# Kernel optimization log

Hardware: AMD Instinct MI355X
Metric: run time of the kernel (lower is better)

## Reference

```python
import jax, jax.numpy as jnp
import numpy as np

B, N = 32, 512
N_DIM, N_P, N_K = 128, 3, 2
F0_DIM = N_DIM * N_P            # 384
CAT_DIM = N_DIM * (N_K + 1) * N_P  # 1152


def setup_inputs() -> dict:
    key = jax.random.key(0)
    ks = jax.random.split(key, 12)
    s = 0.05
    return {
        "loc": jax.random.uniform(ks[0], (B, N, 2), dtype=jnp.float32),
        "deadline": jax.random.uniform(ks[1], (B, N), dtype=jnp.float32),
        "workload": jax.random.uniform(ks[2], (B, N), dtype=jnp.float32),
        "depot": jax.random.uniform(ks[3], (B, 1, 2), dtype=jnp.float32),
        "W_init": jax.random.normal(ks[4], (3, F0_DIM), dtype=jnp.float32) * s,
        "b_init": jnp.zeros((F0_DIM,), jnp.float32),
        "W_dep": jax.random.normal(ks[5], (2, N_DIM), dtype=jnp.float32) * s,
        "b_dep": jnp.zeros((N_DIM,), jnp.float32),
        "W_g1": jax.random.normal(ks[6], (CAT_DIM, N_DIM), dtype=jnp.float32) * s,
        "b_g1": jnp.zeros((N_DIM,), jnp.float32),
        "W_g2": jax.random.normal(ks[7], (CAT_DIM, N_DIM), dtype=jnp.float32) * s,
        "b_g2": jnp.zeros((N_DIM,), jnp.float32),
        "W_g3": jax.random.normal(ks[8], (CAT_DIM, N_DIM), dtype=jnp.float32) * s,
        "b_g3": jnp.zeros((N_DIM,), jnp.float32),
        "gamma": jnp.ones((F0_DIM,), jnp.float32),
        "beta": jnp.zeros((F0_DIM,), jnp.float32),
        "W_F": jax.random.normal(ks[9], (F0_DIM, N_DIM), dtype=jnp.float32) * s,
        "b_F": jnp.zeros((N_DIM,), jnp.float32),
    }


def _forward(loc, deadline, workload, depot, W_init, b_init, W_dep, b_dep,
             W_g1, b_g1, W_g2, b_g2, W_g3, b_g3, gamma, beta, W_F, b_F):
    # X = [loc, deadline/deadline.max()] -> [B,N,3] (workload is concatenated then dropped in original)
    X = jnp.concatenate([loc, (deadline / deadline.max())[..., None]], axis=-1)
    n = X.shape[1]
    # pairwise squared distances [B,N,N]
    d2 = ((X[:, :, None, :] - X[:, None, :, :]) ** 2).sum(-1)
    off = ~jnp.eye(n, dtype=bool)                      # off-diagonal mask
    d2_safe = jnp.where(off, d2, 1.0)
    A = jnp.where(off, 1.0 / jnp.sqrt(d2_safe), 0.0)   # A = 1/dist off-diag, 0 on diag
    A = jnp.where(jnp.isnan(A), 0.0, A)                # A[A!=A]=0
    A = A / A.max()                                    # global max-normalize
    deg = A.sum(-1) - 1.0                              # (A.sum(-1) - 1)
    L = jnp.eye(n, dtype=A.dtype) * deg[:, None, :] - A  # D - A (diag = deg)
    L2 = L @ L

    F0 = X @ W_init + b_init                           # [B,N,384]
    F0_sq = F0 * F0
    F0_cu = F0 * F0_sq

    def prop(F):
        return jnp.concatenate([F, L @ F, L2 @ F], axis=-1)  # [B,N,1152]

    g1 = prop(F0) @ W_g1 + b_g1
    g2 = prop(F0_sq) @ W_g2 + b_g2
    g3 = prop(F0_cu) @ W_g3 + b_g3
    F1 = jnp.concatenate([g1, g2, g3], axis=-1)        # [B,N,384]
    F1 = jax.nn.leaky_relu(F1) + F0

    # BatchNorm1d (training mode): stats over flattened (B*N) samples, biased var
    flat = F1.reshape(-1, F1.shape[-1])
    mu = flat.mean(0)
    var = ((flat - mu) ** 2).mean(0)
    F1 = (F1 - mu) / jnp.sqrt(var + 1e-5) * gamma + beta

    F_final = jax.nn.leaky_relu(F1 @ W_F + b_F)        # [B,N,128]
    dep = depot @ W_dep + b_dep                        # [B,1,128]
    h = jnp.concatenate([dep, F_final], axis=1)        # [B,N+1,128]
    return h, h.mean(axis=1)


def reference(loc, deadline, workload, depot, W_init, b_init, W_dep, b_dep,
              W_g1, b_g1, W_g2, b_g2, W_g3, b_g3, gamma, beta, W_F, b_F):
    return _forward(loc, deadline, workload, depot, W_init, b_init, W_dep, b_dep,
                    W_g1, b_g1, W_g2, b_g2, W_g3, b_g3, gamma, beta, W_F, b_F)
```

## Files before the change

kernel.cpp:

```cpp
#include <hip/hip_runtime.h>

#define LEAKY(x) ((x) > 0.0f ? (x) : 0.01f * (x))

typedef __attribute__((ext_vector_type(8))) short bf16x8;
typedef __attribute__((ext_vector_type(4))) float f32x4;
typedef __attribute__((ext_vector_type(8))) unsigned short u16x8;
typedef __attribute__((ext_vector_type(4))) unsigned short u16x4;

__device__ __forceinline__ unsigned short f2bf(float f) {
    unsigned int u = __float_as_uint(f);
    unsigned int r = (u + 0x7fffu + ((u >> 16) & 1u)) >> 16;
    return (unsigned short)r;
}
__device__ __forceinline__ float bf2f(unsigned short u) {
    return __uint_as_float(((unsigned int)u) << 16);
}

#define GLD16(gp, lp) __builtin_amdgcn_global_load_lds( \
    (__attribute__((address_space(1))) void*)(gp), \
    (__attribute__((address_space(3))) void*)(lp), 16, 0, 0)


__global__ void k_dmax(const float* __restrict__ deadline, float* __restrict__ dmax) {
    __shared__ float red[256];
    int t = threadIdx.x;
    float m = -1e30f;
    for (int i = t; i < 16384; i += 256) m = fmaxf(m, deadline[i]);
    red[t] = m; __syncthreads();
    for (int s = 128; s > 0; s >>= 1) {
        if (t < s) red[t] = fmaxf(red[t], red[t + s]);
        __syncthreads();
    }
    if (t == 0) *dmax = red[0];
}

__global__ __launch_bounds__(256) void k_rowstats(const float* __restrict__ loc,
                                                  const float* __restrict__ deadline,
                                                  const float* __restrict__ dmaxv,
                                                  float* __restrict__ rowsum, float* __restrict__ pmax) {
    int blk = blockIdx.x;
    int wave = threadIdx.x >> 6, lane = threadIdx.x & 63;
    int bi = blk * 4 + wave;
    int b = bi >> 9, i = bi & 511;
    float invd = 1.0f / (*dmaxv);
    const float* lb = loc + b * 1024;
    const float* db = deadline + b * 512;
    float xi = lb[i * 2], yi = lb[i * 2 + 1], zi = db[i] * invd;
    float lsum = 0.f, lmax = 0.f;
    for (int j = lane; j < 512; j += 64) {
        float d0 = xi - lb[j * 2], d1 = yi - lb[j * 2 + 1], d2 = zi - db[j] * invd;
        float dd = d0 * d0 + d1 * d1 + d2 * d2;
        float r = (j == i) ? 0.f : rsqrtf(dd);
        lsum += r; lmax = fmaxf(lmax, r);
    }
    for (int off = 32; off > 0; off >>= 1) {
        lsum += __shfl_down(lsum, off);
        lmax = fmaxf(lmax, __shfl_down(lmax, off));
    }
    __shared__ float smax[4];
    if (lane == 0) { rowsum[bi] = lsum; smax[wave] = lmax; }
    __syncthreads();
    if (threadIdx.x == 0) pmax[blk] = fmaxf(fmaxf(smax[0], smax[1]), fmaxf(smax[2], smax[3]));
}

__global__ void k_amax(const float* __restrict__ pmax, float* __restrict__ amaxf) {
    __shared__ float red[256];
    int t = threadIdx.x;
    float m = 0.f;
    for (int i = t; i < 4096; i += 256) m = fmaxf(m, pmax[i]);
    red[t] = m; __syncthreads();
    for (int s = 128; s > 0; s >>= 1) {
        if (t < s) red[t] = fmaxf(red[t], red[t + s]);
        __syncthreads();
    }
    if (t == 0) *amaxf = red[0];
}

__global__ void k_buildL(const float* __restrict__ loc, const float* __restrict__ deadline,
                         const float* __restrict__ dmaxv, const float* __restrict__ rowsum,
                         const float* __restrict__ amaxf, unsigned short* __restrict__ Lb) {
    int id = blockIdx.x * 256 + threadIdx.x;
    float inv = 1.0f / (*amaxf);
    float invd = 1.0f / (*dmaxv);
    size_t e = (size_t)id * 4;
    size_t bi = e >> 9;
    int b = (int)(bi >> 9);
    int i = (int)(bi & 511);
    int j0 = (int)(e & 511);
    const float* lb = loc + b * 1024;
    const float* db = deadline + b * 512;
    float xi = lb[i * 2], yi = lb[i * 2 + 1], zi = db[i] * invd;
    float4 l01 = *(const float4*)(lb + j0 * 2);
    float4 l23 = *(const float4*)(lb + j0 * 2 + 4);
    float4 dj = *(const float4*)(db + j0);
    float diag = rowsum[bi] * inv - 1.0f;
    float jx[4] = {l01.x, l01.z, l23.x, l23.z};
    float jy[4] = {l01.y, l01.w, l23.y, l23.w};
    float jz[4] = {dj.x * invd, dj.y * invd, dj.z * invd, dj.w * invd};
    u16x4 o;
#pragma unroll
    for (int j = 0; j < 4; j++) {
        float d0 = xi - jx[j], d1 = yi - jy[j], d2 = zi - jz[j];
        float dd = d0 * d0 + d1 * d1 + d2 * d2;
        float v = (i == j0 + j) ? diag : -rsqrtf(dd) * inv;
        o[j] = f2bf(v);
    }
    *(u16x4*)(Lb + e) = o;
}

__global__ void k_F0pow(const float* __restrict__ loc, const float* __restrict__ deadline,
                        const float* __restrict__ dmaxv,
                        const float* __restrict__ Wi, const float* __restrict__ bi_,
                        unsigned short* __restrict__ P1, unsigned short* __restrict__ P2,
                        unsigned short* __restrict__ P3) {
    int id = blockIdx.x * 256 + threadIdx.x;
    int row = id / 96, c4 = (id % 96) * 4;
    float x0 = loc[row * 2], x1 = loc[row * 2 + 1], x2 = deadline[row] / (*dmaxv);
    float4 w0 = *(const float4*)(Wi + c4);
    float4 w1 = *(const float4*)(Wi + 384 + c4);
    float4 w2 = *(const float4*)(Wi + 768 + c4);
    float4 bb = *(const float4*)(bi_ + c4);
    float f[4] = {x0 * w0.x + x1 * w1.x + x2 * w2.x + bb.x,
                  x0 * w0.y + x1 * w1.y + x2 * w2.y + bb.y,
                  x0 * w0.z + x1 * w1.z + x2 * w2.z + bb.z,
                  x0 * w0.w + x1 * w1.w + x2 * w2.w + bb.w};
    u16x4 o1, o2, o3;
#pragma unroll
    for (int j = 0; j < 4; j++) {
        o1[j] = f2bf(f[j]); o2[j] = f2bf(f[j] * f[j]); o3[j] = f2bf(f[j] * f[j] * f[j]);
    }
    size_t e = (size_t)row * 384 + c4;
    *(u16x4*)(P1 + e) = o1; *(u16x4*)(P2 + e) = o2; *(u16x4*)(P3 + e) = o3;
}

__global__ void k_prepW(const float* __restrict__ Wg1, const float* __restrict__ Wg2,
                        const float* __restrict__ Wg3, unsigned short* __restrict__ WgT) {
    int id = blockIdx.x * 256 + threadIdx.x;
    int combo = id / 49152, rem = id % 49152;
    int n = rem / 384, k = rem % 384;
    int kp = combo / 3, part = combo % 3;
    const float* W = (kp == 0) ? Wg1 : (kp == 1 ? Wg2 : Wg3);
    WgT[id] = f2bf(W[(part * 384 + k) * 128 + n]);
}


__device__ __forceinline__ void pipe128x64(
    const unsigned short* __restrict__ A0, int As0, const unsigned short* __restrict__ B0, int Bs0, int it0,
    const unsigned short* __restrict__ A1, int As1, const unsigned short* __restrict__ B1, int Bs1, int it1,
    unsigned short* AsL, unsigned short* BsL,
    f32x4 (&acc)[4][2], int t)
{
    const int lane = t & 63, wave = t >> 6;
    const int wm = wave >> 1, wn = wave & 1;
    const int quad = lane >> 4, l16 = lane & 15;
    const int lrow = lane >> 3;
    const int lsw  = ((lane & 7) ^ lrow) * 8;
    const int total = it0 + it1;

    auto stage = [&](int buf, const unsigned short* A, int As,
                     const unsigned short* B, int Bs, int k0) {
#pragma unroll
        for (int j = 0; j < 4; j++) {
            int r0 = wave * 32 + j * 8;
            GLD16(A + (size_t)(r0 + lrow) * As + k0 + lsw,
                  AsL + buf * 8192 + r0 * 64);
        }
#pragma unroll
        for (int j = 0; j < 2; j++) {
            int r0 = wave * 16 + j * 8;
            GLD16(B + (size_t)(r0 + lrow) * Bs + k0 + lsw,
                  BsL + buf * 4096 + r0 * 64);
        }
    };

    stage(0, A0, As0, B0, Bs0, 0);
    int buf = 0;
    for (int s = 0; s < total; s++) {
        __syncthreads();
        if (s + 1 < total) {
            int s2 = s + 1;
            int sg = (s2 >= it0);
            int k0 = (sg ? (s2 - it0) : s2) * 64;
            stage(buf ^ 1, sg ? A1 : A0, sg ? As1 : As0,
                            sg ? B1 : B0, sg ? Bs1 : Bs0, k0);
        }
#pragma unroll
        for (int h = 0; h < 2; h++) {
            bf16x8 af[4], bfr[2];
            int phys = ((h * 4 + quad) ^ (l16 & 7)) * 8;
#pragma unroll
            for (int i = 0; i < 4; i++)
                af[i] = *(const bf16x8*)(AsL + buf * 8192 + (wm * 64 + i * 16 + l16) * 64 + phys);
#pragma unroll
            for (int n = 0; n < 2; n++)
                bfr[n] = *(const bf16x8*)(BsL + buf * 4096 + (wn * 32 + n * 16 + l16) * 64 + phys);
#pragma unroll
            for (int i = 0; i < 4; i++)
#pragma unroll
                for (int n = 0; n < 2; n++)
                    acc[i][n] = __builtin_amdgcn_mfma_f32_16x16x32_bf16(af[i], bfr[n], acc[i][n], 0, 0, 0);
        }
        buf ^= 1;
    }
}

__device__ __forceinline__ void pipe64x64(
    const unsigned short* __restrict__ A0, int As0, const unsigned short* __restrict__ B0, int Bs0, int it0,
    unsigned short* AsL, unsigned short* BsL,
    f32x4 (&acc)[2][2], int t)
{
    const int lane = t & 63, wave = t >> 6;
    const int wm = wave >> 1, wn = wave & 1;
    const int quad = lane >> 4, l16 = lane & 15;
    const int lrow = lane >> 3;
    const int lsw  = ((lane & 7) ^ lrow) * 8;

    auto stage = [&](int buf, int k0) {
#pragma unroll
        for (int j = 0; j < 2; j++) {
            int r0 = wave * 16 + j * 8;
            GLD16(A0 + (size_t)(r0 + lrow) * As0 + k0 + lsw, AsL + buf * 4096 + r0 * 64);
            GLD16(B0 + (size_t)(r0 + lrow) * Bs0 + k0 + lsw, BsL + buf * 4096 + r0 * 64);
        }
    };

    stage(0, 0);
    int buf = 0;
    for (int s = 0; s < it0; s++) {
        __syncthreads();
        if (s + 1 < it0) stage(buf ^ 1, (s + 1) * 64);
#pragma unroll
        for (int h = 0; h < 2; h++) {
            bf16x8 af[2], bfr[2];
            int phys = ((h * 4 + quad) ^ (l16 & 7)) * 8;
#pragma unroll
            for (int i = 0; i < 2; i++)
                af[i] = *(const bf16x8*)(AsL + buf * 4096 + (wm * 32 + i * 16 + l16) * 64 + phys);
#pragma unroll
            for (int n = 0; n < 2; n++)
                bfr[n] = *(const bf16x8*)(BsL + buf * 4096 + (wn * 32 + n * 16 + l16) * 64 + phys);
#pragma unroll
            for (int i = 0; i < 2; i++)
#pragma unroll
                for (int n = 0; n < 2; n++)
                    acc[i][n] = __builtin_amdgcn_mfma_f32_16x16x32_bf16(af[i], bfr[n], acc[i][n], 0, 0, 0);
        }
        buf ^= 1;
    }
}

__global__ __launch_bounds__(256) void k_ygemmT(
    const unsigned short* __restrict__ WgT,
    const unsigned short* __restrict__ P1, const unsigned short* __restrict__ P2,
    const unsigned short* __restrict__ P3, unsigned short* __restrict__ Y2T)
{
    __shared__ unsigned short AsL[16384], BsL[8192];
    const int t = threadIdx.x;
    const int id = blockIdx.x;
    const int b = id & 31, tt = id >> 5;
    const int kp = tt >> 3, nb = tt & 7;
    const unsigned short* P = (kp == 0) ? P1 : (kp == 1 ? P2 : P3);
    f32x4 acc[4][2];
#pragma unroll
    for (int i = 0; i < 4; i++)
#pragma unroll
        for (int n = 0; n < 2; n++) acc[i][n] = (f32x4){0.f, 0.f, 0.f, 0.f};
    pipe128x64(WgT + (size_t)(kp * 3 + 2) * 49152, 384,
               P + ((size_t)b * 512 + nb * 64) * 384, 384, 6,
               nullptr, 0, nullptr, 0, 0, AsL, BsL, acc, t);

    const int wave = t >> 6, lane = t & 63;
    const int wm = wave >> 1, wn = wave & 1;
    const int quad = lane >> 4, l16 = lane & 15;
#pragma unroll
    for (int i = 0; i < 4; i++)
#pragma unroll
        for (int n = 0; n < 2; n++) {
            int g = kp * 128 + wm * 64 + i * 16 + quad * 4;
            int node = nb * 64 + wn * 32 + n * 16 + l16;
#pragma unroll
            for (int r = 0; r < 4; r++)
                Y2T[((size_t)b * 384 + g + r) * 512 + node] = f2bf(acc[i][n][r]);
        }
}

__global__ __launch_bounds__(256) void k_lg1T(
    const unsigned short* __restrict__ Lb, const unsigned short* __restrict__ Y2T,
    const unsigned short* __restrict__ WgT,
    const unsigned short* __restrict__ P1, const unsigned short* __restrict__ P2,
    const unsigned short* __restrict__ P3, unsigned short* __restrict__ ZT)
{
    __shared__ unsigned short AsL[16384], BsL[8192];
    const int t = threadIdx.x;
    const int id = blockIdx.x;
    const int b = id & 31, tt = id >> 5;
    const int kp = tt >> 3, nb = tt & 7;
    const unsigned short* P = (kp == 0) ? P1 : (kp == 1 ? P2 : P3);
    f32x4 acc[4][2];
#pragma unroll
    for (int i = 0; i < 4; i++)
#pragma unroll
        for (int n = 0; n < 2; n++) acc[i][n] = (f32x4){0.f, 0.f, 0.f, 0.f};
    pipe128x64(Y2T + (size_t)b * 196608 + (size_t)kp * 128 * 512, 512,
               Lb + (size_t)b * 262144 + (size_t)nb * 64 * 512, 512, 8,
               WgT + (size_t)(kp * 3 + 1) * 49152, 384,
               P + ((size_t)b * 512 + nb * 64) * 384, 384, 6, AsL, BsL, acc, t);

    const int wave = t >> 6, lane = t & 63;
    const int wm = wave >> 1, wn = wave & 1;
    const int quad = lane >> 4, l16 = lane & 15;
#pragma unroll
    for (int i = 0; i < 4; i++)
#pragma unroll
        for (int n = 0; n < 2; n++) {
            int g = kp * 128 + wm * 64 + i * 16 + quad * 4;
            int node = nb * 64 + wn * 32 + n * 16 + l16;
#pragma unroll
            for (int r = 0; r < 4; r++)
                ZT[((size_t)b * 384 + g + r) * 512 + node] = f2bf(acc[i][n][r]);
        }
}

__global__ __launch_bounds__(256) void k_lg2(
    const unsigned short* __restrict__ Lb, const unsigned short* __restrict__ ZT,
    const unsigned short* __restrict__ WgT,
    const unsigned short* __restrict__ P1, const unsigned short* __restrict__ P2,
    const unsigned short* __restrict__ P3,
    const float* __restrict__ bg1, const float* __restrict__ bg2, const float* __restrict__ bg3,
    unsigned short* __restrict__ F1b, float* __restrict__ bn1, float* __restrict__ bn2)
{
    __shared__ unsigned short AsL[16384], BsL[8192];
    __shared__ float bnS[64], bnQ[64];
    const int t = threadIdx.x;
    const int id = blockIdx.x;
    const int b = id & 31, tt = id >> 5;
    const int mb = tt & 3, gt = tt >> 2;
    const int kp = gt >> 1;
    if (t < 64) { bnS[t] = 0.f; bnQ[t] = 0.f; }
    const unsigned short* P = (kp == 0) ? P1 : (kp == 1 ? P2 : P3);
    f32x4 acc[4][2];
#pragma unroll
    for (int i = 0; i < 4; i++)
#pragma unroll
        for (int n = 0; n < 2; n++) acc[i][n] = (f32x4){0.f, 0.f, 0.f, 0.f};
    pipe128x64(Lb + (size_t)b * 262144 + (size_t)mb * 128 * 512, 512,
               ZT + (size_t)b * 196608 + (size_t)gt * 64 * 512, 512, 8,
               P + ((size_t)b * 512 + mb * 128) * 384, 384,
               WgT + (size_t)(kp * 3) * 49152 + (size_t)(gt & 1) * 64 * 384, 384, 6,
               AsL, BsL, acc, t);

    const int wave = t >> 6, lane = t & 63;
    const int wm = wave >> 1, wn = wave & 1;
    const int quad = lane >> 4, l16 = lane & 15;
    const float* bg = (kp == 0) ? bg1 : (kp == 1 ? bg2 : bg3);
    float ls1[2], ls2[2];
#pragma unroll
    for (int n = 0; n < 2; n++) { ls1[n] = 0.f; ls2[n] = 0.f; }
#pragma unroll
    for (int i = 0; i < 4; i++) {
        int rowl = mb * 128 + wm * 64 + i * 16 + quad * 4;
        size_t rowg = (size_t)b * 512 + rowl;
#pragma unroll
        for (int n = 0; n < 2; n++) {
            int nloc = wn * 32 + n * 16 + l16;
            int g = gt * 64 + nloc;
            float bias = bg[(gt & 1) * 64 + nloc];
#pragma unroll
            for (int r = 0; r < 4; r++) {
                size_t idx = (rowg + r) * 384 + g;
                float c = acc[i][n][r] + bias;
                float v = LEAKY(c) + bf2f(P1[idx]);
                F1b[idx] = f2bf(v);
                ls1[n] += v; ls2[n] += v * v;
            }
        }
    }
#pragma unroll
    for (int n = 0; n < 2; n++) {
        int nloc = wn * 32 + n * 16 + l16;
        atomicAdd(&bnS[nloc], ls1[n]);
        atomicAdd(&bnQ[nloc], ls2[n]);
    }
    __syncthreads();
    if (t < 64) {
        atomicAdd(&bn1[gt * 64 + t], bnS[t]);
        atomicAdd(&bn2[gt * 64 + t], bnQ[t]);
    }
}

__global__ __launch_bounds__(256) void k_bnfold(
    const float* __restrict__ bn1, const float* __restrict__ bn2,
    const float* __restrict__ gamma, const float* __restrict__ beta,
    const float* __restrict__ WF, const float* __restrict__ bF,
    unsigned short* __restrict__ WFsT, float* __restrict__ beffv)
{
    int blk = blockIdx.x;
    if (blk < 192) {
        int id = blk * 256 + threadIdx.x;
        int n = id / 384, k = id % 384;
        float mu = bn1[k] * (1.f / 16384.f);
        float var = bn2[k] * (1.f / 16384.f) - mu * mu;
        float sc = gamma[k] / sqrtf(var + 1e-5f);
        WFsT[id] = f2bf(WF[k * 128 + n] * sc);
    } else {
        __shared__ float ttL[384];
        int c = threadIdx.x;
        for (int k = c; k < 384; k += 256) {
            float mu = bn1[k] * (1.f / 16384.f);
            float var = bn2[k] * (1.f / 16384.f) - mu * mu;
            float sc = gamma[k] / sqrtf(var + 1e-5f);
            ttL[k] = beta[k] - mu * sc;
        }
        __syncthreads();
        if (c < 128) {
            float a = bF[c];
            for (int k = 0; k < 384; k++) a += ttL[k] * WF[k * 128 + c];
            beffv[c] = a;
        }
    }
}

__global__ __launch_bounds__(256) void k_fgemm(
    const unsigned short* __restrict__ F1b, const unsigned short* __restrict__ WFsT,
    const float* __restrict__ beffv, float* __restrict__ out, float* __restrict__ msum)
{
    __shared__ unsigned short AsL[8192], BsL[8192];
    __shared__ float msS[64];
    const int t = threadIdx.x;
    const int id = blockIdx.x;
    const int b = id & 31, tt = id >> 5;
    const int seg = tt >> 1, nt = tt & 1;
    if (t < 64) msS[t] = 0.f;
    f32x4 acc[2][2];
#pragma unroll
    for (int i = 0; i < 2; i++)
#pragma unroll
        for (int n = 0; n < 2; n++) acc[i][n] = (f32x4){0.f, 0.f, 0.f, 0.f};
    pipe64x64(F1b + ((size_t)b * 512 + seg * 64) * 384, 384,
              WFsT + (size_t)nt * 64 * 384, 384, 6, AsL, BsL, acc, t);

    const int wave = t >> 6, lane = t & 63;
    const int wm = wave >> 1, wn = wave & 1;
    const int quad = lane >> 4, l16 = lane & 15;
    float ls[2];
#pragma unroll
    for (int n = 0; n < 2; n++) ls[n] = 0.f;
#pragma unroll
    for (int i = 0; i < 2; i++) {
        int nd = seg * 64 + wm * 32 + i * 16 + quad * 4;
#pragma unroll
        for (int n = 0; n < 2; n++) {
            int col = nt * 64 + wn * 32 + n * 16 + l16;
            float bb = beffv[col];
#pragma unroll
            for (int r = 0; r < 4; r++) {
                float x = acc[i][n][r] + bb;
                float v = LEAKY(x);
                out[(size_t)b * 65664 + (size_t)(nd + r + 1) * 128 + col] = v;
                ls[n] += v;
            }
        }
    }
#pragma unroll
    for (int n = 0; n < 2; n++) atomicAdd(&msS[wn * 32 + n * 16 + l16], ls[n]);
    __syncthreads();
    if (t < 64) atomicAdd(&msum[b * 128 + nt * 64 + t], msS[t]);
}

__global__ void k_meandep(const float* __restrict__ depot, const float* __restrict__ Wd,
                          const float* __restrict__ bd, const float* __restrict__ msum,
                          float* __restrict__ out) {
    int id = blockIdx.x * 256 + threadIdx.x;
    int b = id >> 7, o = id & 127;
    float dep = depot[b * 2] * Wd[o] + depot[b * 2 + 1] * Wd[128 + o] + bd[o];
    out[(size_t)b * 65664 + o] = dep;
    out[2101248 + id] = (msum[id] + dep) * (1.0f / 513.0f);
}


extern "C" void kernel_launch(void* const* d_in, const int* in_sizes, int n_in,
                              void* d_out, int out_size, void* d_ws, size_t ws_size,
                              hipStream_t stream) {
    const float* loc      = (const float*)d_in[0];
    const float* deadline = (const float*)d_in[1];
    const float* depot    = (const float*)d_in[3];
    const float* W_init   = (const float*)d_in[4];
    const float* b_init   = (const float*)d_in[5];
    const float* W_dep    = (const float*)d_in[6];
    const float* b_dep    = (const float*)d_in[7];
    const float* W_g1     = (const float*)d_in[8];
    const float* b_g1     = (const float*)d_in[9];
    const float* W_g2     = (const float*)d_in[10];
    const float* b_g2     = (const float*)d_in[11];
    const float* W_g3     = (const float*)d_in[12];
    const float* b_g3     = (const float*)d_in[13];
    const float* gamma    = (const float*)d_in[14];
    const float* beta     = (const float*)d_in[15];
    const float* W_F      = (const float*)d_in[16];
    const float* b_F      = (const float*)d_in[17];
    float* out = (float*)d_out;
    float* ws  = (float*)d_ws;

    float* dmaxv  = ws + 0;
    float* amaxf  = ws + 4;
    float* bn1    = ws + 8;
    float* bn2    = ws + 392;
    float* msum   = ws + 776;
    float* rowsum = ws + 4872;
    float* pmax   = ws + 21256;
    float* beffv  = ws + 25736;
    unsigned short* Lb   = (unsigned short*)(ws + 25864);
    unsigned short* P1   = (unsigned short*)(ws + 4220168);
    unsigned short* P2   = (unsigned short*)(ws + 7365896);
    unsigned short* P3   = (unsigned short*)(ws + 10511624);
    unsigned short* WgT  = (unsigned short*)(ws + 13657352);
    unsigned short* WFsT = (unsigned short*)(ws + 13878536);
    unsigned short* Y2T  = (unsigned short*)(ws + 13903112);
    unsigned short* ZT   = (unsigned short*)(ws + 17048840);
    unsigned short* F1b  = (unsigned short*)(ws + 20194568);

    hipMemsetAsync(bn1, 0, (384 + 384 + 4096) * sizeof(float), stream);

    k_dmax<<<1, 256, 0, stream>>>(deadline, dmaxv);
    k_rowstats<<<4096, 256, 0, stream>>>(loc, deadline, dmaxv, rowsum, pmax);
    k_amax<<<1, 256, 0, stream>>>(pmax, amaxf);
    k_buildL<<<8192, 256, 0, stream>>>(loc, deadline, dmaxv, rowsum, amaxf, Lb);
    k_F0pow<<<6144, 256, 0, stream>>>(loc, deadline, dmaxv, W_init, b_init, P1, P2, P3);
    k_prepW<<<1728, 256, 0, stream>>>(W_g1, W_g2, W_g3, WgT);

    k_ygemmT<<<768, 256, 0, stream>>>(WgT, P1, P2, P3, Y2T);
    k_lg1T<<<768, 256, 0, stream>>>(Lb, Y2T, WgT, P1, P2, P3, ZT);
    k_lg2<<<768, 256, 0, stream>>>(Lb, ZT, WgT, P1, P2, P3,
                                   b_g1, b_g2, b_g3, F1b, bn1, bn2);

    k_bnfold<<<193, 256, 0, stream>>>(bn1, bn2, gamma, beta, W_F, b_F, WFsT, beffv);
    k_fgemm<<<512, 256, 0, stream>>>(F1b, WFsT, beffv, out, msum);
    k_meandep<<<16, 256, 0, stream>>>(depot, W_dep, b_dep, msum, out);
}
```

Measured before the change: 236.4 us.

## Enlarge GEMM tiles to 128x128, fuse prep kernels, use atomic max reductions

The three propagation GEMM kernels now use 128x128 output tiles instead of 128x64, which halves the block count and doubles operand reuse per LDS stage. The L-build, F0-power and weight-transpose kernels are merged into one launch, and the WgT layout is reordered so each kp's 128 columns sit contiguously. The single-block max reductions are replaced by multi-block atomicMax on float bits, removing the separate amax kernel. The intent is to cut launch count and raise MFMA density, at the cost of more accumulator registers and LDS per block and only 384 blocks, which may underfill the GPU.

```diff
diff --git a/kernel.cpp b/kernel.cpp
--- a/kernel.cpp
+++ b/kernel.cpp
@@ -22,22 +22,20 @@
 
 
 __global__ void k_dmax(const float* __restrict__ deadline, float* __restrict__ dmax) {
-    __shared__ float red[256];
     int t = threadIdx.x;
-    float m = -1e30f;
-    for (int i = t; i < 16384; i += 256) m = fmaxf(m, deadline[i]);
-    red[t] = m; __syncthreads();
-    for (int s = 128; s > 0; s >>= 1) {
-        if (t < s) red[t] = fmaxf(red[t], red[t + s]);
-        __syncthreads();
-    }
-    if (t == 0) *dmax = red[0];
+    float m = deadline[blockIdx.x * 256 + t];
+    for (int off = 32; off > 0; off >>= 1) m = fmaxf(m, __shfl_down(m, off));
+    __shared__ float s[4];
+    if ((t & 63) == 0) s[t >> 6] = m;
+    __syncthreads();
+    if (t == 0) atomicMax((unsigned int*)dmax,
+                          __float_as_uint(fmaxf(fmaxf(s[0], s[1]), fmaxf(s[2], s[3]))));
 }
 
 __global__ __launch_bounds__(256) void k_rowstats(const float* __restrict__ loc,
                                                   const float* __restrict__ deadline,
                                                   const float* __restrict__ dmaxv,
-                                                  float* __restrict__ rowsum, float* __restrict__ pmax) {
+                                                  float* __restrict__ rowsum, float* __restrict__ pmax64) {
     int blk = blockIdx.x;
     int wave = threadIdx.x >> 6, lane = threadIdx.x & 63;
     int bi = blk * 4 + wave;
@@ -60,95 +58,94 @@
     __shared__ float smax[4];
     if (lane == 0) { rowsum[bi] = lsum; smax[wave] = lmax; }
     __syncthreads();
-    if (threadIdx.x == 0) pmax[blk] = fmaxf(fmaxf(smax[0], smax[1]), fmaxf(smax[2], smax[3]));
-}
-
-__global__ void k_amax(const float* __restrict__ pmax, float* __restrict__ amaxf) {
-    __shared__ float red[256];
+    if (threadIdx.x == 0) {
+        float m = fmaxf(fmaxf(smax[0], smax[1]), fmaxf(smax[2], smax[3]));
+        atomicMax((unsigned int*)(pmax64 + (blk & 63)), __float_as_uint(m));
+    }
+}
+
+__global__ __launch_bounds__(256) void k_build(
+    const float* __restrict__ loc, const float* __restrict__ deadline,
+    const float* __restrict__ dmaxv, const float* __restrict__ rowsum,
+    const float* __restrict__ pmax64,
+    const float* __restrict__ Wi, const float* __restrict__ bi_,
+    const float* __restrict__ Wg1, const float* __restrict__ Wg2, const float* __restrict__ Wg3,
+    unsigned short* __restrict__ Lb,
+    unsigned short* __restrict__ P1, unsigned short* __restrict__ P2, unsigned short* __restrict__ P3,
+    unsigned short* __restrict__ WgT)
+{
+    __shared__ float amaxS;
+    int blk = blockIdx.x;
     int t = threadIdx.x;
-    float m = 0.f;
-    for (int i = t; i < 4096; i += 256) m = fmaxf(m, pmax[i]);
-    red[t] = m; __syncthreads();
-    for (int s = 128; s > 0; s >>= 1) {
-        if (t < s) red[t] = fmaxf(red[t], red[t + s]);
+    if (blk < 8192) {
+        if (t < 64) {
+            float m = pmax64[t];
+            for (int off = 32; off > 0; off >>= 1) m = fmaxf(m, __shfl_down(m, off));
+            if (t == 0) amaxS = m;
+        }
         __syncthreads();
-    }
-    if (t == 0) *amaxf = red[0];
-}
-
-__global__ void k_buildL(const float* __restrict__ loc, const float* __restrict__ deadline,
-                         const float* __restrict__ dmaxv, const float* __restrict__ rowsum,
-                         const float* __restrict__ amaxf, unsigned short* __restrict__ Lb) {
-    int id = blockIdx.x * 256 + threadIdx.x;
-    float inv = 1.0f / (*amaxf);
-    float invd = 1.0f / (*dmaxv);
-    size_t e = (size_t)id * 4;
-    size_t bi = e >> 9;
-    int b = (int)(bi >> 9);
-    int i = (int)(bi & 511);
-    int j0 = (int)(e & 511);
-    const float* lb = loc + b * 1024;
-    const float* db = deadline + b * 512;
-    float xi = lb[i * 2], yi = lb[i * 2 + 1], zi = db[i] * invd;
-    float4 l01 = *(const float4*)(lb + j0 * 2);
-    float4 l23 = *(const float4*)(lb + j0 * 2 + 4);
-    float4 dj = *(const float4*)(db + j0);
-    float diag = rowsum[bi] * inv - 1.0f;
-    float jx[4] = {l01.x, l01.z, l23.x, l23.z};
-    float jy[4] = {l01.y, l01.w, l23.y, l23.w};
-    float jz[4] = {dj.x * invd, dj.y * invd, dj.z * invd, dj.w * invd};
-    u16x4 o;
-#pragma unroll
-    for (int j = 0; j < 4; j++) {
-        float d0 = xi - jx[j], d1 = yi - jy[j], d2 = zi - jz[j];
-        float dd = d0 * d0 + d1 * d1 + d2 * d2;
-        float v = (i == j0 + j) ? diag : -rsqrtf(dd) * inv;
-        o[j] = f2bf(v);
-    }
-    *(u16x4*)(Lb + e) = o;
-}
-
-__global__ void k_F0pow(const float* __restrict__ loc, const float* __restrict__ deadline,
-                        const float* __restrict__ dmaxv,
-                        const float* __restrict__ Wi, const float* __restrict__ bi_,
-                        unsigned short* __restrict__ P1, unsigned short* __restrict__ P2,
-                        unsigned short* __restrict__ P3) {
-    int id = blockIdx.x * 256 + threadIdx.x;
-    int row = id / 96, c4 = (id % 96) * 4;
-    float x0 = loc[row * 2], x1 = loc[row * 2 + 1], x2 = deadline[row] / (*dmaxv);
-    float4 w0 = *(const float4*)(Wi + c4);
-    float4 w1 = *(const float4*)(Wi + 384 + c4);
-    float4 w2 = *(const float4*)(Wi + 768 + c4);
-    float4 bb = *(const float4*)(bi_ + c4);
-    float f[4] = {x0 * w0.x + x1 * w1.x + x2 * w2.x + bb.x,
-                  x0 * w0.y + x1 * w1.y + x2 * w2.y + bb.y,
-                  x0 * w0.z + x1 * w1.z + x2 * w2.z + bb.z,
-                  x0 * w0.w + x1 * w1.w + x2 * w2.w + bb.w};
-    u16x4 o1, o2, o3;
-#pragma unroll
-    for (int j = 0; j < 4; j++) {
-        o1[j] = f2bf(f[j]); o2[j] = f2bf(f[j] * f[j]); o3[j] = f2bf(f[j] * f[j] * f[j]);
-    }
-    size_t e = (size_t)row * 384 + c4;
-    *(u16x4*)(P1 + e) = o1; *(u16x4*)(P2 + e) = o2; *(u16x4*)(P3 + e) = o3;
-}
-
-__global__ void k_prepW(const float* __restrict__ Wg1, const float* __restrict__ Wg2,
-                        const float* __restrict__ Wg3, unsigned short* __restrict__ WgT) {
-    int id = blockIdx.x * 256 + threadIdx.x;
-    int combo = id / 49152, rem = id % 49152;
-    int n = rem / 384, k = rem % 384;
-    int kp = combo / 3, part = combo % 3;
-    const float* W = (kp == 0) ? Wg1 : (kp == 1 ? Wg2 : Wg3);
-    WgT[id] = f2bf(W[(part * 384 + k) * 128 + n]);
-}
-
-
-__device__ __forceinline__ void pipe128x64(
+        float inv = 1.0f / amaxS;
+        float invd = 1.0f / (*dmaxv);
+        int id = blk * 256 + t;
+        size_t e = (size_t)id * 4;
+        size_t bi = e >> 9;
+        int b = (int)(bi >> 9);
+        int i = (int)(bi & 511);
+        int j0 = (int)(e & 511);
+        const float* lb = loc + b * 1024;
+        const float* db = deadline + b * 512;
+        float xi = lb[i * 2], yi = lb[i * 2 + 1], zi = db[i] * invd;
+        float4 l01 = *(const float4*)(lb + j0 * 2);
+        float4 l23 = *(const float4*)(lb + j0 * 2 + 4);
+        float4 dj = *(const float4*)(db + j0);
+        float diag = rowsum[bi] * inv - 1.0f;
+        float jx[4] = {l01.x, l01.z, l23.x, l23.z};
+        float jy[4] = {l01.y, l01.w, l23.y, l23.w};
+        float jz[4] = {dj.x * invd, dj.y * invd, dj.z * invd, dj.w * invd};
+        u16x4 o;
+#pragma unroll
+        for (int j = 0; j < 4; j++) {
+            float d0 = xi - jx[j], d1 = yi - jy[j], d2 = zi - jz[j];
+            float dd = d0 * d0 + d1 * d1 + d2 * d2;
+            float v = (i == j0 + j) ? diag : -rsqrtf(dd) * inv;
+            o[j] = f2bf(v);
+        }
+        *(u16x4*)(Lb + e) = o;
+    } else if (blk < 14336) {
+        int id = (blk - 8192) * 256 + t;
+        int row = id / 96, c4 = (id % 96) * 4;
+        float x0 = loc[row * 2], x1 = loc[row * 2 + 1], x2 = deadline[row] / (*dmaxv);
+        float4 w0 = *(const float4*)(Wi + c4);
+        float4 w1 = *(const float4*)(Wi + 384 + c4);
+        float4 w2 = *(const float4*)(Wi + 768 + c4);
+        float4 bb = *(const float4*)(bi_ + c4);
+        float f[4] = {x0 * w0.x + x1 * w1.x + x2 * w2.x + bb.x,
+                      x0 * w0.y + x1 * w1.y + x2 * w2.y + bb.y,
+                      x0 * w0.z + x1 * w1.z + x2 * w2.z + bb.z,
+                      x0 * w0.w + x1 * w1.w + x2 * w2.w + bb.w};
+        u16x4 o1, o2, o3;
+#pragma unroll
+        for (int j = 0; j < 4; j++) {
+            o1[j] = f2bf(f[j]); o2[j] = f2bf(f[j] * f[j]); o3[j] = f2bf(f[j] * f[j] * f[j]);
+        }
+        size_t e = (size_t)row * 384 + c4;
+        *(u16x4*)(P1 + e) = o1; *(u16x4*)(P2 + e) = o2; *(u16x4*)(P3 + e) = o3;
+    } else {
+        int id = (blk - 14336) * 256 + t;
+        int part = id / 147456, rem = id % 147456;
+        int g = rem / 384, k = rem % 384;
+        int kp = g >> 7, n = g & 127;
+        const float* W = (kp == 0) ? Wg1 : (kp == 1 ? Wg2 : Wg3);
+        WgT[id] = f2bf(W[(part * 384 + k) * 128 + n]);
+    }
+}
+
+
+__device__ __forceinline__ void pipe128x128(
     const unsigned short* __restrict__ A0, int As0, const unsigned short* __restrict__ B0, int Bs0, int it0,
     const unsigned short* __restrict__ A1, int As1, const unsigned short* __restrict__ B1, int Bs1, int it1,
     unsigned short* AsL, unsigned short* BsL,
-    f32x4 (&acc)[4][2], int t)
+    f32x4 (&acc)[4][4], int t)
 {
     const int lane = t & 63, wave = t >> 6;
     const int wm = wave >> 1, wn = wave & 1;
@@ -162,14 +159,8 @@
 #pragma unroll
         for (int j = 0; j < 4; j++) {
             int r0 = wave * 32 + j * 8;
-            GLD16(A + (size_t)(r0 + lrow) * As + k0 + lsw,
-                  AsL + buf * 8192 + r0 * 64);
-        }
-#pragma unroll
-        for (int j = 0; j < 2; j++) {
-            int r0 = wave * 16 + j * 8;
-            GLD16(B + (size_t)(r0 + lrow) * Bs + k0 + lsw,
-                  BsL + buf * 4096 + r0 * 64);
+            GLD16(A + (size_t)(r0 + lrow) * As + k0 + lsw, AsL + buf * 8192 + r0 * 64);
+            GLD16(B + (size_t)(r0 + lrow) * Bs + k0 + lsw, BsL + buf * 8192 + r0 * 64);
         }
     };
 
@@ -186,18 +177,18 @@
         }
 #pragma unroll
         for (int h = 0; h < 2; h++) {
-            bf16x8 af[4], bfr[2];
+            bf16x8 af[4], bfr[4];
             int phys = ((h * 4 + quad) ^ (l16 & 7)) * 8;
 #pragma unroll
             for (int i = 0; i < 4; i++)
                 af[i] = *(const bf16x8*)(AsL + buf * 8192 + (wm * 64 + i * 16 + l16) * 64 + phys);
 #pragma unroll
-            for (int n = 0; n < 2; n++)
-                bfr[n] = *(const bf16x8*)(BsL + buf * 4096 + (wn * 32 + n * 16 + l16) * 64 + phys);
+            for (int n = 0; n < 4; n++)
+                bfr[n] = *(const bf16x8*)(BsL + buf * 8192 + (wn * 64 + n * 16 + l16) * 64 + phys);
 #pragma unroll
             for (int i = 0; i < 4; i++)
 #pragma unroll
-                for (int n = 0; n < 2; n++)
+                for (int n = 0; n < 4; n++)
                     acc[i][n] = __builtin_amdgcn_mfma_f32_16x16x32_bf16(af[i], bfr[n], acc[i][n], 0, 0, 0);
         }
         buf ^= 1;
@@ -254,20 +245,20 @@
     const unsigned short* __restrict__ P1, const unsigned short* __restrict__ P2,
     const unsigned short* __restrict__ P3, unsigned short* __restrict__ Y2T)
 {
-    __shared__ unsigned short AsL[16384], BsL[8192];
+    __shared__ unsigned short AsL[16384], BsL[16384];
     const int t = threadIdx.x;
     const int id = blockIdx.x;
     const int b = id & 31, tt = id >> 5;
-    const int kp = tt >> 3, nb = tt & 7;
+    const int kp = tt >> 2, nb = tt & 3;
     const unsigned short* P = (kp == 0) ? P1 : (kp == 1 ? P2 : P3);
-    f32x4 acc[4][2];
+    f32x4 acc[4][4];
 #pragma unroll
     for (int i = 0; i < 4; i++)
 #pragma unroll
-        for (int n = 0; n < 2; n++) acc[i][n] = (f32x4){0.f, 0.f, 0.f, 0.f};
-    pipe128x64(WgT + (size_t)(kp * 3 + 2) * 49152, 384,
-               P + ((size_t)b * 512 + nb * 64) * 384, 384, 6,
-               nullptr, 0, nullptr, 0, 0, AsL, BsL, acc, t);
+        for (int n = 0; n < 4; n++) acc[i][n] = (f32x4){0.f, 0.f, 0.f, 0.f};
+    pipe128x128(WgT + ((size_t)2 * 384 + kp * 128) * 384, 384,
+                P + ((size_t)b * 512 + nb * 128) * 384, 384, 6,
+                nullptr, 0, nullptr, 0, 0, AsL, BsL, acc, t);
 
     const int wave = t >> 6, lane = t & 63;
     const int wm = wave >> 1, wn = wave & 1;
@@ -275,9 +266,9 @@
 #pragma unroll
     for (int i = 0; i < 4; i++)
 #pragma unroll
-        for (int n = 0; n < 2; n++) {
+        for (int n = 0; n < 4; n++) {
             int g = kp * 128 + wm * 64 + i * 16 + quad * 4;
-            int node = nb * 64 + wn * 32 + n * 16 + l16;
+            int node = nb * 128 + wn * 64 + n * 16 + l16;
 #pragma unroll
             for (int r = 0; r < 4; r++)
                 Y2T[((size_t)b * 384 + g + r) * 512 + node] = f2bf(acc[i][n][r]);
@@ -290,21 +281,21 @@
     const unsigned short* __restrict__ P1, const unsigned short* __restrict__ P2,
     const unsigned short* __restrict__ P3, unsigned short* __restrict__ ZT)
 {
-    __shared__ unsigned short AsL[16384], BsL[8192];
+    __shared__ unsigned short AsL[16384], BsL[16384];
     const int t = threadIdx.x;
     const int id = blockIdx.x;
     const int b = id & 31, tt = id >> 5;
-    const int kp = tt >> 3, nb = tt & 7;
+    const int kp = tt >> 2, nb = tt & 3;
     const unsigned short* P = (kp == 0) ? P1 : (kp == 1 ? P2 : P3);
-    f32x4 acc[4][2];
+    f32x4 acc[4][4];
 #pragma unroll
     for (int i = 0; i < 4; i++)
 #pragma unroll
-        for (int n = 0; n < 2; n++) acc[i][n] = (f32x4){0.f, 0.f, 0.f, 0.f};
-    pipe128x64(Y2T + (size_t)b * 196608 + (size_t)kp * 128 * 512, 512,
-               Lb + (size_t)b * 262144 + (size_t)nb * 64 * 512, 512, 8,
-               WgT + (size_t)(kp * 3 + 1) * 49152, 384,
-               P + ((size_t)b * 512 + nb * 64) * 384, 384, 6, AsL, BsL, acc, t);
+        for (int n = 0; n < 4; n++) acc[i][n] = (f32x4){0.f, 0.f, 0.f, 0.f};
+    pipe128x128(Y2T + (size_t)b * 196608 + (size_t)kp * 128 * 512, 512,
+                Lb + (size_t)b * 262144 + (size_t)nb * 128 * 512, 512, 8,
+                WgT + ((size_t)1 * 384 + kp * 128) * 384, 384,
+                P + ((size_t)b * 512 + nb * 128) * 384, 384, 6, AsL, BsL, acc, t);
 
     const int wave = t >> 6, lane = t & 63;
     const int wm = wave >> 1, wn = wave & 1;
@@ -312,9 +303,9 @@
 #pragma unroll
     for (int i = 0; i < 4; i++)
 #pragma unroll
-        for (int n = 0; n < 2; n++) {
+        for (int n = 0; n < 4; n++) {
             int g = kp * 128 + wm * 64 + i * 16 + quad * 4;
-            int node = nb * 64 + wn * 32 + n * 16 + l16;
+            int node = nb * 128 + wn * 64 + n * 16 + l16;
 #pragma unroll
             for (int r = 0; r < 4; r++)
                 ZT[((size_t)b * 384 + g + r) * 512 + node] = f2bf(acc[i][n][r]);
@@ -329,42 +320,41 @@
     const float* __restrict__ bg1, const float* __restrict__ bg2, const float* __restrict__ bg3,
     unsigned short* __restrict__ F1b, float* __restrict__ bn1, float* __restrict__ bn2)
 {
-    __shared__ unsigned short AsL[16384], BsL[8192];
-    __shared__ float bnS[64], bnQ[64];
+    __shared__ unsigned short AsL[16384], BsL[16384];
+    __shared__ float bnS[128], bnQ[128];
     const int t = threadIdx.x;
     const int id = blockIdx.x;
     const int b = id & 31, tt = id >> 5;
     const int mb = tt & 3, gt = tt >> 2;
-    const int kp = gt >> 1;
-    if (t < 64) { bnS[t] = 0.f; bnQ[t] = 0.f; }
-    const unsigned short* P = (kp == 0) ? P1 : (kp == 1 ? P2 : P3);
-    f32x4 acc[4][2];
+    if (t < 128) { bnS[t] = 0.f; bnQ[t] = 0.f; }
+    const unsigned short* P = (gt == 0) ? P1 : (gt == 1 ? P2 : P3);
+    f32x4 acc[4][4];
 #pragma unroll
     for (int i = 0; i < 4; i++)
 #pragma unroll
-        for (int n = 0; n < 2; n++) acc[i][n] = (f32x4){0.f, 0.f, 0.f, 0.f};
-    pipe128x64(Lb + (size_t)b * 262144 + (size_t)mb * 128 * 512, 512,
-               ZT + (size_t)b * 196608 + (size_t)gt * 64 * 512, 512, 8,
-               P + ((size_t)b * 512 + mb * 128) * 384, 384,
-               WgT + (size_t)(kp * 3) * 49152 + (size_t)(gt & 1) * 64 * 384, 384, 6,
-               AsL, BsL, acc, t);
+        for (int n = 0; n < 4; n++) acc[i][n] = (f32x4){0.f, 0.f, 0.f, 0.f};
+    pipe128x128(Lb + (size_t)b * 262144 + (size_t)mb * 128 * 512, 512,
+                ZT + (size_t)b * 196608 + (size_t)gt * 128 * 512, 512, 8,
+                P + ((size_t)b * 512 + mb * 128) * 384, 384,
+                WgT + (size_t)(gt * 128) * 384, 384, 6,
+                AsL, BsL, acc, t);
 
     const int wave = t >> 6, lane = t & 63;
     const int wm = wave >> 1, wn = wave & 1;
     const int quad = lane >> 4, l16 = lane & 15;
-    const float* bg = (kp == 0) ? bg1 : (kp == 1 ? bg2 : bg3);
-    float ls1[2], ls2[2];
-#pragma unroll
-    for (int n = 0; n < 2; n++) { ls1[n] = 0.f; ls2[n] = 0.f; }
+    const float* bg = (gt == 0) ? bg1 : (gt == 1 ? bg2 : bg3);
+    float ls1[4], ls2[4];
+#pragma unroll
+    for (int n = 0; n < 4; n++) { ls1[n] = 0.f; ls2[n] = 0.f; }
 #pragma unroll
     for (int i = 0; i < 4; i++) {
         int rowl = mb * 128 + wm * 64 + i * 16 + quad * 4;
         size_t rowg = (size_t)b * 512 + rowl;
 #pragma unroll
-        for (int n = 0; n < 2; n++) {
-            int nloc = wn * 32 + n * 16 + l16;
-            int g = gt * 64 + nloc;
-            float bias = bg[(gt & 1) * 64 + nloc];
+        for (int n = 0; n < 4; n++) {
+            int nloc = wn * 64 + n * 16 + l16;
+            int g = gt * 128 + nloc;
+            float bias = bg[nloc];
 #pragma unroll
             for (int r = 0; r < 4; r++) {
                 size_t idx = (rowg + r) * 384 + g;
@@ -376,15 +366,15 @@
         }
     }
 #pragma unroll
-    for (int n = 0; n < 2; n++) {
-        int nloc = wn * 32 + n * 16 + l16;
+    for (int n = 0; n < 4; n++) {
+        int nloc = wn * 64 + n * 16 + l16;
         atomicAdd(&bnS[nloc], ls1[n]);
         atomicAdd(&bnQ[nloc], ls2[n]);
     }
     __syncthreads();
-    if (t < 64) {
-        atomicAdd(&bn1[gt * 64 + t], bnS[t]);
-        atomicAdd(&bn2[gt * 64 + t], bnQ[t]);
+    if (t < 128) {
+        atomicAdd(&bn1[gt * 128 + t], bnS[t]);
+        atomicAdd(&bn2[gt * 128 + t], bnQ[t]);
     }
 }
 
@@ -502,35 +492,33 @@
     float* ws  = (float*)d_ws;
 
     float* dmaxv  = ws + 0;
-    float* amaxf  = ws + 4;
-    float* bn1    = ws + 8;
-    float* bn2    = ws + 392;
-    float* msum   = ws + 776;
-    float* rowsum = ws + 4872;
-    float* pmax   = ws + 21256;
-    float* beffv  = ws + 25736;
-    unsigned short* Lb   = (unsigned short*)(ws + 25864);
-    unsigned short* P1   = (unsigned short*)(ws + 4220168);
-    unsigned short* P2   = (unsigned short*)(ws + 7365896);
-    unsigned short* P3   = (unsigned short*)(ws + 10511624);
-    unsigned short* WgT  = (unsigned short*)(ws + 13657352);
-    unsigned short* WFsT = (unsigned short*)(ws + 13878536);
-    unsigned short* Y2T  = (unsigned short*)(ws + 13903112);
-    unsigned short* ZT   = (unsigned short*)(ws + 17048840);
-    unsigned short* F1b  = (unsigned short*)(ws + 20194568);
-
-    hipMemsetAsync(bn1, 0, (384 + 384 + 4096) * sizeof(float), stream);
-
-    k_dmax<<<1, 256, 0, stream>>>(deadline, dmaxv);
-    k_rowstats<<<4096, 256, 0, stream>>>(loc, deadline, dmaxv, rowsum, pmax);
-    k_amax<<<1, 256, 0, stream>>>(pmax, amaxf);
-    k_buildL<<<8192, 256, 0, stream>>>(loc, deadline, dmaxv, rowsum, amaxf, Lb);
-    k_F0pow<<<6144, 256, 0, stream>>>(loc, deadline, dmaxv, W_init, b_init, P1, P2, P3);
-    k_prepW<<<1728, 256, 0, stream>>>(W_g1, W_g2, W_g3, WgT);
-
-    k_ygemmT<<<768, 256, 0, stream>>>(WgT, P1, P2, P3, Y2T);
-    k_lg1T<<<768, 256, 0, stream>>>(Lb, Y2T, WgT, P1, P2, P3, ZT);
-    k_lg2<<<768, 256, 0, stream>>>(Lb, ZT, WgT, P1, P2, P3,
+    float* pmax64 = ws + 4;
+    float* bn1    = ws + 68;
+    float* bn2    = ws + 452;
+    float* msum   = ws + 836;
+    float* rowsum = ws + 4932;
+    float* beffv  = ws + 21316;
+    unsigned short* Lb   = (unsigned short*)(ws + 21448);
+    unsigned short* P1   = (unsigned short*)(ws + 4215752);
+    unsigned short* P2   = (unsigned short*)(ws + 7361480);
+    unsigned short* P3   = (unsigned short*)(ws + 10507208);
+    unsigned short* WgT  = (unsigned short*)(ws + 13652936);
+    unsigned short* WFsT = (unsigned short*)(ws + 13874120);
+    unsigned short* Y2T  = (unsigned short*)(ws + 13898696);
+    unsigned short* ZT   = (unsigned short*)(ws + 17044424);
+    unsigned short* F1b  = (unsigned short*)(ws + 20190152);
+
+    hipMemsetAsync(ws, 0, 4932 * sizeof(float), stream);
+
+    k_dmax<<<64, 256, 0, stream>>>(deadline, dmaxv);
+    k_rowstats<<<4096, 256, 0, stream>>>(loc, deadline, dmaxv, rowsum, pmax64);
+    k_build<<<16064, 256, 0, stream>>>(loc, deadline, dmaxv, rowsum, pmax64,
+                                       W_init, b_init, W_g1, W_g2, W_g3,
+                                       Lb, P1, P2, P3, WgT);
+
+    k_ygemmT<<<384, 256, 0, stream>>>(WgT, P1, P2, P3, Y2T);
+    k_lg1T<<<384, 256, 0, stream>>>(Lb, Y2T, WgT, P1, P2, P3, ZT);
+    k_lg2<<<384, 256, 0, stream>>>(Lb, ZT, WgT, P1, P2, P3,
                                    b_g1, b_g2, b_g3, F1b, bn1, bn2);
 
     k_bnfold<<<193, 256, 0, stream>>>(bn1, bn2, gamma, beta, W_F, b_F, WFsT, beffv);
```

Measured after the change: 241.4 us. 2.1% more time.
